# Kernel tuning notes

Hardware: AMD Instinct MI355X
Metric: run time of the kernel (lower is better)

The kernel has to match this reference:

```python
import jax, jax.numpy as jnp
import numpy as np

B = 65536          # users in batch
N_USERS = 200000
N_ENTITY = 100000
D = 64             # n_factors
N_RK = 3
LEAKY_SLOPE = 0.2


def setup_inputs() -> dict:
    key = jax.random.key(0)
    ks = jax.random.split(key, 8)
    rng = np.random.default_rng(0)
    # ragged lengths per user (>=1 so no empty segments)
    len_a = rng.integers(1, 80, size=B)
    len_c = rng.integers(1, 20, size=B)
    seg_a = jnp.asarray(np.repeat(np.arange(B), len_a), dtype=jnp.int32)
    seg_c = jnp.asarray(np.repeat(np.arange(B), len_c), dtype=jnp.int32)
    Ta, Tc = int(len_a.sum()), int(len_c.sum())
    return {
        "user_id": jax.random.randint(ks[0], (B,), 0, N_USERS),
        "artists_ids": jax.random.randint(ks[1], (Ta,), 0, N_ENTITY),
        "artists_seg": seg_a,
        "categories_ids": jax.random.randint(ks[2], (Tc,), 0, N_ENTITY),
        "categories_seg": seg_c,
        "user_factors": jax.random.normal(ks[3], (N_USERS, D), dtype=jnp.float32),
        "entity_factors": jax.random.normal(ks[4], (N_ENTITY, D), dtype=jnp.float32),
        "relation_k": jax.random.normal(ks[5], (D, N_RK), dtype=jnp.float32),
    }


def reference(user_id, artists_ids, artists_seg, categories_ids, categories_seg,
              user_factors, entity_factors, relation_k):
    users = user_factors[user_id]                                  # [B, D]
    # aspect importance: leaky_relu(U @ Rk) -> softmax over n_rk
    scores = jax.nn.softmax(
        jax.nn.leaky_relu(users @ relation_k, LEAKY_SLOPE), axis=1)  # [B, 3]

    def contrib(ids, seg):
        # ragged gather + per-item dot + segment mean (== calculate_score)
        d = jnp.einsum('td,td->t', entity_factors[ids], users[seg])  # [T]
        s = jax.ops.segment_sum(d, seg, num_segments=B)
        cnt = jax.ops.segment_sum(jnp.ones_like(d), seg, num_segments=B)
        return s / cnt

    c_a = contrib(artists_ids, artists_seg)        # contribute_actors [B]
    c_c = contrib(categories_ids, categories_seg)  # contribute_directors [B]

    s_a, s_c = scores[:, 0], scores[:, 1]
    prediction = (c_a * s_a + c_c * s_c) / (s_a + s_c)
    return (prediction, scores, c_a, c_c)
```

## Files before the change

### kernel.cpp

```cpp
#include <hip/hip_runtime.h>

#define NB 65536
#define D 64
#define SLOPE 0.2f

typedef _Float16 h2f __attribute__((ext_vector_type(2)));

__device__ __forceinline__ h2f as_h2(unsigned x) {
    union { unsigned u; h2f h; } v; v.u = x; return v.h;
}

struct UH { h2f h0, h1, h2, h3; };

__device__ __forceinline__ float dot8(uint4 w, const UH& u, float acc) {
#if __has_builtin(__builtin_amdgcn_fdot2)
    acc = __builtin_amdgcn_fdot2(as_h2(w.x), u.h0, acc, false);
    acc = __builtin_amdgcn_fdot2(as_h2(w.y), u.h1, acc, false);
    acc = __builtin_amdgcn_fdot2(as_h2(w.z), u.h2, acc, false);
    acc = __builtin_amdgcn_fdot2(as_h2(w.w), u.h3, acc, false);
#else
    h2f t0 = as_h2(w.x) * u.h0 + as_h2(w.y) * u.h1;
    h2f t1 = as_h2(w.z) * u.h2 + as_h2(w.w) * u.h3;
    acc += (float)t0.x + (float)t0.y + (float)t1.x + (float)t1.y;
#endif
    return acc;
}

__device__ __forceinline__ float reduce8(float v) {
#pragma unroll
    for (int off = 1; off <= 4; off <<= 1)
        v += __shfl_xor(v, off, 64);
    return v;
}
__device__ __forceinline__ float reduce64(float v) {
#pragma unroll
    for (int off = 1; off <= 32; off <<= 1)
        v += __shfl_xor(v, off, 64);
    return v;
}

__device__ __forceinline__ int lower_bound(const int* __restrict__ seg, int n, int key) {
    int lo = 0, hi = n;
    while (lo < hi) {
        int mid = (lo + hi) >> 1;
        if (seg[mid] < key) lo = mid + 1;
        else hi = mid;
    }
    return lo;
}

__global__ __launch_bounds__(256)
void prepass(const float2* __restrict__ ef2, unsigned* __restrict__ eh, int n2,
             const int* __restrict__ a_seg, int Ta, int* __restrict__ offs_a,
             const int* __restrict__ c_seg, int Tc, int* __restrict__ offs_c)
{
    const int t = blockIdx.x * blockDim.x + threadIdx.x;
    if (t < n2) {
        float2 v = ef2[t];
        h2f h = { (_Float16)v.x, (_Float16)v.y };
        union { h2f h; unsigned u; } cv; cv.h = h;
        eh[t] = cv.u;
    }
    if (t < Ta) {
        int s = a_seg[t];
        if (t == 0) offs_a[0] = 0;
        else if (a_seg[t - 1] != s) offs_a[s] = t;
        if (t == Ta - 1) offs_a[s + 1] = Ta;
    }
    if (t < Tc) {
        int s = c_seg[t];
        if (t == 0) offs_c[0] = 0;
        else if (c_seg[t - 1] != s) offs_c[s] = t;
        if (t == Tc - 1) offs_c[s + 1] = Tc;
    }
}

template<int MODE>
__global__ __launch_bounds__(256)
void aspect_kernel(const int* __restrict__ user_id,
                   const int* __restrict__ a_ids, const int* __restrict__ a_seg,
                   const int* __restrict__ offs_a, int Ta,
                   const int* __restrict__ c_ids, const int* __restrict__ c_seg,
                   const int* __restrict__ offs_c, int Tc,
                   const float* __restrict__ user_factors,
                   const float4* __restrict__ ef4,
                   const uint4* __restrict__ efh,
                   const float* __restrict__ relation_k,
                   float* __restrict__ out)
{
    const int wave = (blockIdx.x * blockDim.x + threadIdx.x) >> 6;
    const int lane = threadIdx.x & 63;
    const int r = lane >> 3;
    const int c = lane & 7;
    const int b = wave;

    const int uid = user_id[b];
    const float4 ua = reinterpret_cast<const float4*>(user_factors)[uid * 16 + 2 * c];
    const float4 ub = reinterpret_cast<const float4*>(user_factors)[uid * 16 + 2 * c + 1];

    float p0 = 0.f, p1 = 0.f, p2 = 0.f;
    {
        const float uv[8] = {ua.x, ua.y, ua.z, ua.w, ub.x, ub.y, ub.z, ub.w};
#pragma unroll
        for (int j = 0; j < 8; ++j) {
            const int row = 8 * c + j;
            p0 += uv[j] * relation_k[row * 3 + 0];
            p1 += uv[j] * relation_k[row * 3 + 1];
            p2 += uv[j] * relation_k[row * 3 + 2];
        }
    }
    float l0 = reduce8(p0), l1 = reduce8(p1), l2 = reduce8(p2);
    l0 = l0 > 0.f ? l0 : SLOPE * l0;
    l1 = l1 > 0.f ? l1 : SLOPE * l1;
    l2 = l2 > 0.f ? l2 : SLOPE * l2;
    const float m  = fmaxf(l0, fmaxf(l1, l2));
    const float e0 = __expf(l0 - m);
    const float e1 = __expf(l1 - m);
    const float e2 = __expf(l2 - m);
    const float inv = 1.0f / (e0 + e1 + e2);
    const float s0 = e0 * inv, s1 = e1 * inv, s2 = e2 * inv;

    int sa, ea, sc, ec;
    if (MODE == 1) {
        sa = offs_a[b]; ea = offs_a[b + 1];
        sc = offs_c[b]; ec = offs_c[b + 1];
    } else {
        sa = lower_bound(a_seg, Ta, b); ea = lower_bound(a_seg, Ta, b + 1);
        sc = lower_bound(c_seg, Tc, b); ec = lower_bound(c_seg, Tc, b + 1);
    }

    UH uh;
    uh.h0 = h2f{ (_Float16)ua.x, (_Float16)ua.y };
    uh.h1 = h2f{ (_Float16)ua.z, (_Float16)ua.w };
    uh.h2 = h2f{ (_Float16)ub.x, (_Float16)ub.y };
    uh.h3 = h2f{ (_Float16)ub.z, (_Float16)ub.w };

    auto gather_dot_f16 = [&](const int* __restrict__ ids, int s, int e) -> float {
        float acc = 0.f;
        int t = s;
        for (; t + 16 <= e; t += 16) {
            const int id0 = ids[t + r];
            const int id1 = ids[t + 8 + r];
            const uint4 w0 = efh[id0 * 8 + c];
            const uint4 w1 = efh[id1 * 8 + c];
            acc = dot8(w0, uh, acc);
            acc = dot8(w1, uh, acc);
        }
        if (t + r < e) {
            const uint4 w0 = efh[ids[t + r] * 8 + c];
            acc = dot8(w0, uh, acc);
        }
        t += 8;
        if (t < e && t + r < e) {
            const uint4 w1 = efh[ids[t + r] * 8 + c];
            acc = dot8(w1, uh, acc);
        }
        return reduce64(acc);
    };

    auto gather_dot_f32 = [&](const int* __restrict__ ids, int s, int e) -> float {
        const int g = lane >> 4, k = lane & 15;
        const float4 u4 = reinterpret_cast<const float4*>(user_factors)[uid * 16 + k];
        float ax = 0.f, ay = 0.f, az = 0.f, aw = 0.f;
        int t = s;
        for (; t + 4 <= e; t += 4) {
            const int i0 = ids[t + g];
            const float4 v0 = ef4[i0 * 16 + k];
            ax += v0.x; ay += v0.y; az += v0.z; aw += v0.w;
        }
        if (t + g < e) {
            const int i0 = ids[t + g];
            const float4 v0 = ef4[i0 * 16 + k];
            ax += v0.x; ay += v0.y; az += v0.z; aw += v0.w;
        }
        const float part = ax * u4.x + ay * u4.y + az * u4.z + aw * u4.w;
        return reduce64(part);
    };

    float c_a, c_c;
    if (MODE == 1) {
        c_a = gather_dot_f16(a_ids, sa, ea) / (float)(ea - sa);
        c_c = gather_dot_f16(c_ids, sc, ec) / (float)(ec - sc);
    } else {
        c_a = gather_dot_f32(a_ids, sa, ea) / (float)(ea - sa);
        c_c = gather_dot_f32(c_ids, sc, ec) / (float)(ec - sc);
    }

    const float pred = (c_a * s0 + c_c * s1) / (s0 + s1);

    if (lane == 0) {
        out[b]          = pred;
        out[4 * NB + b] = c_a;
        out[5 * NB + b] = c_c;
    }
    if (lane < 3) {
        const float sv = (lane == 0) ? s0 : ((lane == 1) ? s1 : s2);
        out[NB + 3 * b + lane] = sv;
    }
}

extern "C" void kernel_launch(void* const* d_in, const int* in_sizes, int n_in,
                              void* d_out, int out_size, void* d_ws, size_t ws_size,
                              hipStream_t stream) {
    const int*   user_id        = (const int*)d_in[0];
    const int*   artists_ids    = (const int*)d_in[1];
    const int*   artists_seg    = (const int*)d_in[2];
    const int*   categories_ids = (const int*)d_in[3];
    const int*   categories_seg = (const int*)d_in[4];
    const float* user_factors   = (const float*)d_in[5];
    const float* entity_factors = (const float*)d_in[6];
    const float* relation_k     = (const float*)d_in[7];
    float* out = (float*)d_out;

    const int Ta = in_sizes[1];
    const int Tc = in_sizes[3];
    const int n_ent_elems = in_sizes[6];
    const int n2 = n_ent_elems / 2;

    const size_t table_bytes = (size_t)n_ent_elems * 2;
    const size_t offs_bytes  = (size_t)2 * (NB + 1) * sizeof(int);
    const int blocks = NB / 4;

    if (ws_size >= table_bytes + offs_bytes) {
        unsigned* efh   = (unsigned*)d_ws;
        int*      offs_a = (int*)((unsigned char*)d_ws + table_bytes);
        int*      offs_c = offs_a + (NB + 1);
        int prep_n = n2 > Ta ? n2 : Ta;
        if (Tc > prep_n) prep_n = Tc;
        prepass<<<(prep_n + 255) / 256, 256, 0, stream>>>(
            (const float2*)entity_factors, efh, n2,
            artists_seg, Ta, offs_a,
            categories_seg, Tc, offs_c);
        aspect_kernel<1><<<blocks, 256, 0, stream>>>(user_id,
            artists_ids, artists_seg, offs_a, Ta,
            categories_ids, categories_seg, offs_c, Tc,
            user_factors, (const float4*)entity_factors, (const uint4*)efh,
            relation_k, out);
    } else {
        aspect_kernel<0><<<blocks, 256, 0, stream>>>(user_id,
            artists_ids, artists_seg, nullptr, Ta,
            categories_ids, categories_seg, nullptr, Tc,
            user_factors, (const float4*)entity_factors, nullptr,
            relation_k, out);
    }
}
```

Baseline: 77.15 us.

## Split each user's ragged segments across two waves and combine via shared memory

The main kernel now assigns two wavefronts per user, each gathering and dotting half of the artist and category items. Partial sums are exchanged through shared memory after a block barrier, and only the first wave computes the softmax and writes outputs. This doubles wave-level parallelism and shortens each wave's serial gather loop, which is meant to cut tail latency on long segments. The cost is twice as many waves doing fixed setup work, a __syncthreads, and idle second waves during the epilogue. The fallback path is refactored into its own kernel.

```diff
diff --git a/kernel.cpp b/kernel.cpp
--- a/kernel.cpp
+++ b/kernel.cpp
@@ -75,59 +75,27 @@
     }
 }
 
-template<int MODE>
 __global__ __launch_bounds__(256)
-void aspect_kernel(const int* __restrict__ user_id,
-                   const int* __restrict__ a_ids, const int* __restrict__ a_seg,
-                   const int* __restrict__ offs_a, int Ta,
-                   const int* __restrict__ c_ids, const int* __restrict__ c_seg,
-                   const int* __restrict__ offs_c, int Tc,
-                   const float* __restrict__ user_factors,
-                   const float4* __restrict__ ef4,
-                   const uint4* __restrict__ efh,
-                   const float* __restrict__ relation_k,
-                   float* __restrict__ out)
+void aspect_pair(const int* __restrict__ user_id,
+                 const int* __restrict__ a_ids, const int* __restrict__ offs_a,
+                 const int* __restrict__ c_ids, const int* __restrict__ offs_c,
+                 const float* __restrict__ user_factors,
+                 const uint4* __restrict__ efh,
+                 const float* __restrict__ relation_k,
+                 float* __restrict__ out)
 {
-    const int wave = (blockIdx.x * blockDim.x + threadIdx.x) >> 6;
-    const int lane = threadIdx.x & 63;
+    const int tid  = threadIdx.x;
+    const int wib  = tid >> 6;
+    const int lane = tid & 63;
+    const int pair = wib >> 1;
+    const int half = wib & 1;
+    const int b    = blockIdx.x * 2 + pair;
     const int r = lane >> 3;
     const int c = lane & 7;
-    const int b = wave;
 
     const int uid = user_id[b];
     const float4 ua = reinterpret_cast<const float4*>(user_factors)[uid * 16 + 2 * c];
     const float4 ub = reinterpret_cast<const float4*>(user_factors)[uid * 16 + 2 * c + 1];
-
-    float p0 = 0.f, p1 = 0.f, p2 = 0.f;
-    {
-        const float uv[8] = {ua.x, ua.y, ua.z, ua.w, ub.x, ub.y, ub.z, ub.w};
-#pragma unroll
-        for (int j = 0; j < 8; ++j) {
-            const int row = 8 * c + j;
-            p0 += uv[j] * relation_k[row * 3 + 0];
-            p1 += uv[j] * relation_k[row * 3 + 1];
-            p2 += uv[j] * relation_k[row * 3 + 2];
-        }
-    }
-    float l0 = reduce8(p0), l1 = reduce8(p1), l2 = reduce8(p2);
-    l0 = l0 > 0.f ? l0 : SLOPE * l0;
-    l1 = l1 > 0.f ? l1 : SLOPE * l1;
-    l2 = l2 > 0.f ? l2 : SLOPE * l2;
-    const float m  = fmaxf(l0, fmaxf(l1, l2));
-    const float e0 = __expf(l0 - m);
-    const float e1 = __expf(l1 - m);
-    const float e2 = __expf(l2 - m);
-    const float inv = 1.0f / (e0 + e1 + e2);
-    const float s0 = e0 * inv, s1 = e1 * inv, s2 = e2 * inv;
-
-    int sa, ea, sc, ec;
-    if (MODE == 1) {
-        sa = offs_a[b]; ea = offs_a[b + 1];
-        sc = offs_c[b]; ec = offs_c[b + 1];
-    } else {
-        sa = lower_bound(a_seg, Ta, b); ea = lower_bound(a_seg, Ta, b + 1);
-        sc = lower_bound(c_seg, Tc, b); ec = lower_bound(c_seg, Tc, b + 1);
-    }
 
     UH uh;
     uh.h0 = h2f{ (_Float16)ua.x, (_Float16)ua.y };
@@ -135,7 +103,15 @@
     uh.h2 = h2f{ (_Float16)ub.x, (_Float16)ub.y };
     uh.h3 = h2f{ (_Float16)ub.z, (_Float16)ub.w };
 
-    auto gather_dot_f16 = [&](const int* __restrict__ ids, int s, int e) -> float {
+    const int sa = offs_a[b], ea = offs_a[b + 1];
+    const int sc = offs_c[b], ec = offs_c[b + 1];
+
+    const int ma = sa + ((ea - sa + 1) >> 1);
+    const int mc = sc + ((ec - sc + 1) >> 1);
+    const int s_a = half ? ma : sa, e_a = half ? ea : ma;
+    const int s_c = half ? mc : sc, e_c = half ? ec : mc;
+
+    auto gather = [&](const int* __restrict__ ids, int s, int e) -> float {
         float acc = 0.f;
         int t = s;
         for (; t + 16 <= e; t += 16) {
@@ -158,34 +134,111 @@
         return reduce64(acc);
     };
 
-    auto gather_dot_f32 = [&](const int* __restrict__ ids, int s, int e) -> float {
-        const int g = lane >> 4, k = lane & 15;
-        const float4 u4 = reinterpret_cast<const float4*>(user_factors)[uid * 16 + k];
+    const float pa = gather(a_ids, s_a, e_a);
+    const float pc = gather(c_ids, s_c, e_c);
+
+    __shared__ float xch[4][2];
+    if (lane == 0) { xch[wib][0] = pa; xch[wib][1] = pc; }
+    __syncthreads();
+
+    if (half == 0) {
+        float p0 = 0.f, p1 = 0.f, p2 = 0.f;
+        {
+            const float uv[8] = {ua.x, ua.y, ua.z, ua.w, ub.x, ub.y, ub.z, ub.w};
+#pragma unroll
+            for (int j = 0; j < 8; ++j) {
+                const int row = 8 * c + j;
+                p0 += uv[j] * relation_k[row * 3 + 0];
+                p1 += uv[j] * relation_k[row * 3 + 1];
+                p2 += uv[j] * relation_k[row * 3 + 2];
+            }
+        }
+        float l0 = reduce8(p0), l1 = reduce8(p1), l2 = reduce8(p2);
+        l0 = l0 > 0.f ? l0 : SLOPE * l0;
+        l1 = l1 > 0.f ? l1 : SLOPE * l1;
+        l2 = l2 > 0.f ? l2 : SLOPE * l2;
+        const float m  = fmaxf(l0, fmaxf(l1, l2));
+        const float e0 = __expf(l0 - m);
+        const float e1 = __expf(l1 - m);
+        const float e2 = __expf(l2 - m);
+        const float inv = 1.0f / (e0 + e1 + e2);
+        const float s0 = e0 * inv, s1 = e1 * inv, s2 = e2 * inv;
+
+        const float c_a = (xch[2 * pair][0] + xch[2 * pair + 1][0]) / (float)(ea - sa);
+        const float c_c = (xch[2 * pair][1] + xch[2 * pair + 1][1]) / (float)(ec - sc);
+        const float pred = (c_a * s0 + c_c * s1) / (s0 + s1);
+
+        if (lane == 0) {
+            out[b]          = pred;
+            out[4 * NB + b] = c_a;
+            out[5 * NB + b] = c_c;
+        }
+        if (lane < 3) {
+            const float sv = (lane == 0) ? s0 : ((lane == 1) ? s1 : s2);
+            out[NB + 3 * b + lane] = sv;
+        }
+    }
+}
+
+__global__ __launch_bounds__(256)
+void aspect_fallback(const int* __restrict__ user_id,
+                     const int* __restrict__ a_ids, const int* __restrict__ a_seg, int Ta,
+                     const int* __restrict__ c_ids, const int* __restrict__ c_seg, int Tc,
+                     const float* __restrict__ user_factors,
+                     const float4* __restrict__ ef4,
+                     const float* __restrict__ relation_k,
+                     float* __restrict__ out)
+{
+    const int b    = blockIdx.x * 4 + (threadIdx.x >> 6);
+    const int lane = threadIdx.x & 63;
+    const int g = lane >> 4, k = lane & 15;
+
+    const int uid = user_id[b];
+    const float4 u4 = reinterpret_cast<const float4*>(user_factors)[uid * 16 + k];
+
+    float p0 = 0.f, p1 = 0.f, p2 = 0.f;
+    {
+        const float uv[4] = {u4.x, u4.y, u4.z, u4.w};
+#pragma unroll
+        for (int j = 0; j < 4; ++j) {
+            const int row = 4 * k + j;
+            p0 += uv[j] * relation_k[row * 3 + 0];
+            p1 += uv[j] * relation_k[row * 3 + 1];
+            p2 += uv[j] * relation_k[row * 3 + 2];
+        }
+    }
+#pragma unroll
+    for (int off = 1; off <= 8; off <<= 1) {
+        p0 += __shfl_xor(p0, off, 64);
+        p1 += __shfl_xor(p1, off, 64);
+        p2 += __shfl_xor(p2, off, 64);
+    }
+    float l0 = p0 > 0.f ? p0 : SLOPE * p0;
+    float l1 = p1 > 0.f ? p1 : SLOPE * p1;
+    float l2 = p2 > 0.f ? p2 : SLOPE * p2;
+    const float m  = fmaxf(l0, fmaxf(l1, l2));
+    const float e0 = __expf(l0 - m), e1 = __expf(l1 - m), e2 = __expf(l2 - m);
+    const float inv = 1.0f / (e0 + e1 + e2);
+    const float s0 = e0 * inv, s1 = e1 * inv, s2 = e2 * inv;
+
+    auto gd = [&](const int* __restrict__ ids, int s, int e) -> float {
         float ax = 0.f, ay = 0.f, az = 0.f, aw = 0.f;
         int t = s;
         for (; t + 4 <= e; t += 4) {
-            const int i0 = ids[t + g];
-            const float4 v0 = ef4[i0 * 16 + k];
+            const float4 v0 = ef4[ids[t + g] * 16 + k];
             ax += v0.x; ay += v0.y; az += v0.z; aw += v0.w;
         }
         if (t + g < e) {
-            const int i0 = ids[t + g];
-            const float4 v0 = ef4[i0 * 16 + k];
+            const float4 v0 = ef4[ids[t + g] * 16 + k];
             ax += v0.x; ay += v0.y; az += v0.z; aw += v0.w;
         }
-        const float part = ax * u4.x + ay * u4.y + az * u4.z + aw * u4.w;
-        return reduce64(part);
+        return reduce64(ax * u4.x + ay * u4.y + az * u4.z + aw * u4.w);
     };
 
-    float c_a, c_c;
-    if (MODE == 1) {
-        c_a = gather_dot_f16(a_ids, sa, ea) / (float)(ea - sa);
-        c_c = gather_dot_f16(c_ids, sc, ec) / (float)(ec - sc);
-    } else {
-        c_a = gather_dot_f32(a_ids, sa, ea) / (float)(ea - sa);
-        c_c = gather_dot_f32(c_ids, sc, ec) / (float)(ec - sc);
-    }
-
+    const int sa = lower_bound(a_seg, Ta, b), ea = lower_bound(a_seg, Ta, b + 1);
+    const int sc = lower_bound(c_seg, Tc, b), ec = lower_bound(c_seg, Tc, b + 1);
+    const float c_a = gd(a_ids, sa, ea) / (float)(ea - sa);
+    const float c_c = gd(c_ids, sc, ec) / (float)(ec - sc);
     const float pred = (c_a * s0 + c_c * s1) / (s0 + s1);
 
     if (lane == 0) {
@@ -219,10 +272,9 @@
 
     const size_t table_bytes = (size_t)n_ent_elems * 2;
     const size_t offs_bytes  = (size_t)2 * (NB + 1) * sizeof(int);
-    const int blocks = NB / 4;
 
     if (ws_size >= table_bytes + offs_bytes) {
-        unsigned* efh   = (unsigned*)d_ws;
+        unsigned* efh    = (unsigned*)d_ws;
         int*      offs_a = (int*)((unsigned char*)d_ws + table_bytes);
         int*      offs_c = offs_a + (NB + 1);
         int prep_n = n2 > Ta ? n2 : Ta;
@@ -231,16 +283,13 @@
             (const float2*)entity_factors, efh, n2,
             artists_seg, Ta, offs_a,
             categories_seg, Tc, offs_c);
-        aspect_kernel<1><<<blocks, 256, 0, stream>>>(user_id,
-            artists_ids, artists_seg, offs_a, Ta,
-            categories_ids, categories_seg, offs_c, Tc,
-            user_factors, (const float4*)entity_factors, (const uint4*)efh,
-            relation_k, out);
+        aspect_pair<<<NB / 2, 256, 0, stream>>>(user_id,
+            artists_ids, offs_a, categories_ids, offs_c,
+            user_factors, (const uint4*)efh, relation_k, out);
     } else {
-        aspect_kernel<0><<<blocks, 256, 0, stream>>>(user_id,
-            artists_ids, artists_seg, nullptr, Ta,
-            categories_ids, categories_seg, nullptr, Tc,
-            user_factors, (const float4*)entity_factors, nullptr,
-            relation_k, out);
-    }
-}
+        aspect_fallback<<<NB / 4, 256, 0, stream>>>(user_id,
+            artists_ids, artists_seg, Ta,
+            categories_ids, categories_seg, Tc,
+            user_factors, (const float4*)entity_factors, relation_k, out);
+    }
+}
```

Result: slower. 99.40 us (+28.8%).
